# Optimization experiments

Hardware: AMD Instinct MI355X
Metric: run time of the kernel (lower is better)

The kernel has to match this reference:

```python
import jax, jax.numpy as jnp
import numpy as np

B, T, I, H, R, O = 128, 512, 64, 512, 4, 64
NOISE_STD = 0.05
TAU = 0.2


def setup_inputs() -> dict:
    key = jax.random.key(0)
    ks = jax.random.split(key, 16)
    s = 0.08  # xavier-ish scale to keep gates in sane range
    return {
        "u": jax.random.normal(ks[0], (B, T, I), jnp.float32),
        "x0": jnp.zeros((B, H), jnp.float32),
        "noise": jax.random.normal(ks[1], (T, B, H), jnp.float32),
        "W_ir": jax.random.normal(ks[2], (H, I), jnp.float32) * s,
        "b_ir": jax.random.normal(ks[3], (H,), jnp.float32) * s,
        "W_iz": jax.random.normal(ks[4], (H, I), jnp.float32) * s,
        "b_iz": jax.random.normal(ks[5], (H,), jnp.float32) * s,
        "W_ih": jax.random.normal(ks[6], (H, I), jnp.float32) * s,
        "b_ih": jax.random.normal(ks[7], (H,), jnp.float32) * s,
        "N_hr": jax.random.normal(ks[8], (H, R), jnp.float32) * s,
        "M_hr": jax.random.normal(ks[9], (H, R), jnp.float32) * s,
        "N_hz": jax.random.normal(ks[10], (H, R), jnp.float32) * s,
        "M_hz": jax.random.normal(ks[11], (H, R), jnp.float32) * s,
        "N_hh": jax.random.normal(ks[12], (H, R), jnp.float32) * s,
        "M_hh": jax.random.normal(ks[13], (H, R), jnp.float32) * s,
        "W_out": jax.random.normal(ks[14], (O, H), jnp.float32) * s,
        "b_out": jax.random.normal(ks[15], (O,), jnp.float32) * s,
    }


def reference(u, x0, noise, W_ir, b_ir, W_iz, b_iz, W_ih, b_ih,
              N_hr, M_hr, N_hz, M_hz, N_hh, M_hh, W_out, b_out):
    scale = 1.0 / u.shape[-1] * 0 + 1.0 / N_hr.shape[0]  # 1/H (cont mode)
    scale = 1.0 / N_hr.shape[0]
    u_t = jnp.transpose(u, (1, 0, 2))  # [T,B,I]
    # precompute input projections for all steps (same math as per-step Linear)
    ir = jnp.einsum('tbi,hi->tbh', u_t, W_ir) + b_ir
    iz = jnp.einsum('tbi,hi->tbh', u_t, W_iz) + b_iz
    ih = jnp.einsum('tbi,hi->tbh', u_t, W_ih) + b_ih

    def step(x, inp):
        ir_t, iz_t, ih_t, n_t = inp
        hr = (x @ N_hr) @ M_hr.T * scale
        hz = (x @ N_hz) @ M_hz.T * scale
        r = jax.nn.sigmoid(ir_t + hr)
        z = jax.nn.sigmoid(iz_t + hz)
        hh = ((r * x) @ N_hh) @ M_hh.T * scale
        g = jnp.tanh(ih_t + hh)
        rec_x = (1.0 - z) * g + z * x
        x_new = x + NOISE_STD * n_t + TAU * (-x + rec_x)  # cont mode
        return x_new, x_new

    x_last, traj = jax.lax.scan(step, x0, (ir, iz, ih, noise))  # traj: [T,B,H]
    traj = jnp.transpose(traj, (1, 0, 2))  # [B,T,H]
    output = jnp.einsum('bth,oh->bto', traj, W_out) + b_out
    return output, x_last, traj
```

## Files before the change

### kernel.cpp

```cpp
#include <hip/hip_runtime.h>
#include <hip/hip_bf16.h>
#include <stdint.h>

#define Bv 128
#define Tv 512
#define Iv 64
#define Hv 512
#define Ov 64

typedef __attribute__((ext_vector_type(8))) short bv8;
typedef __attribute__((ext_vector_type(4))) float fv4;
typedef __attribute__((ext_vector_type(4))) unsigned uv4;
typedef __attribute__((ext_vector_type(2))) unsigned uv2;
typedef __attribute__((ext_vector_type(8))) unsigned short usv8;

#define LOG2E 1.44269504f
#define TWOLOG2E 2.88539008f

static __device__ __forceinline__ unsigned short f2bf(float f) {
  unsigned u = __builtin_bit_cast(unsigned, f);
  u += 0x7fffu + ((u >> 16) & 1u);
  return (unsigned short)(u >> 16);
}
static __device__ __forceinline__ float bf2f(unsigned short s) {
  return __builtin_bit_cast(float, ((unsigned)s) << 16);
}

template <int CTRL>
static __device__ __forceinline__ float dpp_add(float v) {
  int t = __builtin_amdgcn_update_dpp(0, __builtin_bit_cast(int, v), CTRL, 0xF, 0xF, true);
  return v + __builtin_bit_cast(float, t);
}

static __device__ __forceinline__ float wave_red(float v) {
  v = dpp_add<0xB1>(v);
  v = dpp_add<0x4E>(v);
  v = dpp_add<0x124>(v);
  v = dpp_add<0x128>(v);
  unsigned a = __builtin_bit_cast(unsigned, v);
  uv2 p = __builtin_amdgcn_permlane16_swap(a, a, false, false);
  v = __builtin_bit_cast(float, p[0]) + __builtin_bit_cast(float, p[1]);
  a = __builtin_bit_cast(unsigned, v);
  uv2 q = __builtin_amdgcn_permlane32_swap(a, a, false, false);
  v = __builtin_bit_cast(float, q[0]) + __builtin_bit_cast(float, q[1]);
  return v;
}

__global__ __launch_bounds__(256) void proj_kernel(
    const float* __restrict__ u,
    const float* __restrict__ Wir, const float* __restrict__ bir,
    const float* __restrict__ Wiz, const float* __restrict__ biz,
    const float* __restrict__ Wih, const float* __restrict__ bih,
    unsigned* __restrict__ irz, unsigned short* __restrict__ ihb)
{
  __shared__ __align__(16) unsigned short As[64][72];
  const int bt0 = blockIdx.x * 64;
  const int h0b = blockIdx.y * 64;
  const int tid = threadIdx.x;
  {
    const int r = tid >> 2, ksg = (tid & 3) * 16;
    const float* src = u + (size_t)(bt0 + r) * Iv + ksg;
    unsigned short tmp[16];
#pragma unroll
    for (int i = 0; i < 16; i += 4) {
      float4 v = *(const float4*)(src + i);
      tmp[i] = f2bf(v.x); tmp[i+1] = f2bf(v.y); tmp[i+2] = f2bf(v.z); tmp[i+3] = f2bf(v.w);
    }
    *(uv4*)&As[r][ksg]     = *(uv4*)&tmp[0];
    *(uv4*)&As[r][ksg + 8] = *(uv4*)&tmp[8];
  }
  __syncthreads();
  const int wave = tid >> 6, lane = tid & 63;
  const int n = lane & 15, q = lane >> 4;
  const int h = h0b + wave * 16 + n;
  const float* Wg[3] = {Wir, Wiz, Wih};
  const float SCL[3] = {LOG2E, LOG2E, TWOLOG2E};
  bv8 bfrag[3][2];
#pragma unroll
  for (int g = 0; g < 3; ++g)
#pragma unroll
    for (int ks = 0; ks < 2; ++ks) {
      const float* wp = Wg[g] + (size_t)h * Iv + ks * 32 + q * 8;
      float4 w0 = *(const float4*)wp, w1 = *(const float4*)(wp + 4);
      const float s = SCL[g];
      bv8 f;
      f[0] = (short)f2bf(w0.x * s); f[1] = (short)f2bf(w0.y * s);
      f[2] = (short)f2bf(w0.z * s); f[3] = (short)f2bf(w0.w * s);
      f[4] = (short)f2bf(w1.x * s); f[5] = (short)f2bf(w1.y * s);
      f[6] = (short)f2bf(w1.z * s); f[7] = (short)f2bf(w1.w * s);
      bfrag[g][ks] = f;
    }
  const float bs0 = bir[h] * LOG2E, bs1 = biz[h] * LOG2E, bs2 = bih[h] * TWOLOG2E;
#pragma unroll
  for (int sub = 0; sub < 4; ++sub) {
    bv8 a0 = *(const bv8*)&As[sub * 16 + n][q * 8];
    bv8 a1 = *(const bv8*)&As[sub * 16 + n][32 + q * 8];
    fv4 ar = {0.f,0.f,0.f,0.f}, az = {0.f,0.f,0.f,0.f}, ah = {0.f,0.f,0.f,0.f};
    ar = __builtin_amdgcn_mfma_f32_16x16x32_bf16(a0, bfrag[0][0], ar, 0, 0, 0);
    ar = __builtin_amdgcn_mfma_f32_16x16x32_bf16(a1, bfrag[0][1], ar, 0, 0, 0);
    az = __builtin_amdgcn_mfma_f32_16x16x32_bf16(a0, bfrag[1][0], az, 0, 0, 0);
    az = __builtin_amdgcn_mfma_f32_16x16x32_bf16(a1, bfrag[1][1], az, 0, 0, 0);
    ah = __builtin_amdgcn_mfma_f32_16x16x32_bf16(a0, bfrag[2][0], ah, 0, 0, 0);
    ah = __builtin_amdgcn_mfma_f32_16x16x32_bf16(a1, bfrag[2][1], ah, 0, 0, 0);
#pragma unroll
    for (int j = 0; j < 4; ++j) {
      const int row = bt0 + sub * 16 + q * 4 + j;
      const size_t slot = (size_t)row * Hv + h;
      irz[slot] = ((unsigned)f2bf(az[j] + bs1) << 16) | (unsigned)f2bf(ar[j] + bs0);
      ihb[slot] = f2bf(ah[j] + bs2);
    }
  }
}

struct Buf { uv4 irz0, irz1; usv8 ih; fv4 nz0, nz1; };
#define IRZ(bf, j) ((j) < 4 ? (bf).irz0[(j)] : (bf).irz1[(j) - 4])
#define NZE(bf, j) ((j) < 4 ? (bf).nz0[(j)]  : (bf).nz1[(j) - 4])

__global__ __launch_bounds__(64, 1) void scan_kernel(
    const float* __restrict__ x0, const float* __restrict__ noise,
    const float* __restrict__ Nhr, const float* __restrict__ Mhr,
    const float* __restrict__ Nhz, const float* __restrict__ Mhz,
    const float* __restrict__ Nhh, const float* __restrict__ Mhh,
    unsigned* __restrict__ traj, const unsigned short* __restrict__ ihb,
    float* __restrict__ xlast)
{
  const int b = blockIdx.x, lane = threadIdx.x;
  const int h0 = lane * 8;
  const float scr = (1.0f / 512.0f) * LOG2E;
  const float sch = (1.0f / 512.0f) * TWOLOG2E;
  fv4 nr[8], nz_[8], nh[8], mr[8], mz[8], mh[8];
#pragma unroll
  for (int j = 0; j < 8; ++j) {
    nr[j]  = *(const fv4*)(Nhr + (size_t)(h0 + j) * 4);
    nz_[j] = *(const fv4*)(Nhz + (size_t)(h0 + j) * 4);
    nh[j]  = *(const fv4*)(Nhh + (size_t)(h0 + j) * 4);
    mr[j]  = *(const fv4*)(Mhr + (size_t)(h0 + j) * 4) * scr;
    mz[j]  = *(const fv4*)(Mhz + (size_t)(h0 + j) * 4) * scr;
    mh[j]  = *(const fv4*)(Mhh + (size_t)(h0 + j) * 4) * sch;
  }
#pragma unroll
  for (int j = 0; j < 8; ++j) {
    asm("" : "+a"(nr[j]), "+a"(nz_[j]), "+a"(nh[j]));
    asm("" : "+a"(mr[j]), "+a"(mz[j]), "+a"(mh[j]));
  }
  float x[8];
  {
    fv4 a = *(const fv4*)(x0 + (size_t)b * Hv + h0);
    fv4 c = *(const fv4*)(x0 + (size_t)b * Hv + h0 + 4);
#pragma unroll
    for (int j = 0; j < 4; ++j) { x[j] = a[j]; x[j + 4] = c[j]; }
  }
  const size_t rowbase = (size_t)b * Tv * Hv + h0;
  const size_t nbase = (size_t)b * Hv + h0;
  Buf A, Bb;
  auto LOAD = [&](Buf& bf, int t) {
    const unsigned* p = traj + rowbase + (size_t)t * Hv;
    bf.irz0 = *(const uv4*)p;
    bf.irz1 = *(const uv4*)(p + 4);
    bf.ih = *(const usv8*)(ihb + rowbase + (size_t)t * Hv);
    const float* np = noise + (size_t)t * (Bv * Hv) + nbase;
    bf.nz0 = *(const fv4*)np;
    bf.nz1 = *(const fv4*)(np + 4);
  };
  auto STEP = [&](const Buf& bf, int t) {
    float sr[4] = {0, 0, 0, 0}, sz[4] = {0, 0, 0, 0};
#pragma unroll
    for (int j = 0; j < 8; ++j)
#pragma unroll
      for (int r = 0; r < 4; ++r) {
        sr[r] = fmaf(x[j], nr[j][r], sr[r]);
        sz[r] = fmaf(x[j], nz_[j][r], sz[r]);
      }
#pragma unroll
    for (int r = 0; r < 4; ++r) { sr[r] = wave_red(sr[r]); sz[r] = wave_red(sz[r]); }
    float rx[8], zz[8];
#pragma unroll
    for (int j = 0; j < 8; ++j) {
      float hr = fmaf(sr[3], mr[j][3], fmaf(sr[2], mr[j][2], fmaf(sr[1], mr[j][1], sr[0] * mr[j][0])));
      float hz = fmaf(sz[3], mz[j][3], fmaf(sz[2], mz[j][2], fmaf(sz[1], mz[j][1], sz[0] * mz[j][0])));
      unsigned w = IRZ(bf, j);
      float irv = __builtin_bit_cast(float, w << 16);
      float izv = __builtin_bit_cast(float, w & 0xffff0000u);
      float er = __builtin_amdgcn_exp2f(-(irv + hr));
      float ez = __builtin_amdgcn_exp2f(-(izv + hz));
      rx[j] = __builtin_amdgcn_rcpf(1.0f + er) * x[j];
      zz[j] = __builtin_amdgcn_rcpf(1.0f + ez);
    }
    float sh[4] = {0, 0, 0, 0};
#pragma unroll
    for (int j = 0; j < 8; ++j)
#pragma unroll
      for (int r = 0; r < 4; ++r) sh[r] = fmaf(rx[j], nh[j][r], sh[r]);
#pragma unroll
    for (int r = 0; r < 4; ++r) sh[r] = wave_red(sh[r]);
#pragma unroll
    for (int j = 0; j < 8; ++j) {
      float hh = fmaf(sh[3], mh[j][3], fmaf(sh[2], mh[j][2], fmaf(sh[1], mh[j][1], sh[0] * mh[j][0])));
      float a = fmaxf(bf2f(bf.ih[j]) + hh, -44.0f);
      float e = __builtin_amdgcn_exp2f(-a);
      float g = (1.f - e) * __builtin_amdgcn_rcpf(1.f + e);
      x[j] = x[j] + 0.05f * NZE(bf, j) + 0.2f * (1.f - zz[j]) * (g - x[j]);
    }
    float* op = (float*)(traj + rowbase + (size_t)t * Hv);
    fv4 s0 = {x[0], x[1], x[2], x[3]}, s1 = {x[4], x[5], x[6], x[7]};
    *(fv4*)op = s0;
    *(fv4*)(op + 4) = s1;
  };
  LOAD(A, 0);
  for (int t = 0; t < Tv; t += 2) {
    LOAD(Bb, t + 1);
    STEP(A, t);
    if (t + 2 < Tv) LOAD(A, t + 2);
    STEP(Bb, t + 1);
  }
  {
    fv4 s0 = {x[0], x[1], x[2], x[3]}, s1 = {x[4], x[5], x[6], x[7]};
    *(fv4*)(xlast + nbase) = s0;
    *(fv4*)(xlast + nbase + 4) = s1;
  }
}

__global__ __launch_bounds__(256) void outproj_kernel(
    const float* __restrict__ traj, const float* __restrict__ Wout,
    const float* __restrict__ bout, float* __restrict__ out)
{
  __shared__ __align__(16) unsigned short As[64][40];
  const int bt0 = blockIdx.x * 64;
  const int tid = threadIdx.x;
  const int wave = tid >> 6, lane = tid & 63;
  const int n = lane & 15, q = lane >> 4;
  const int o = wave * 16 + n;
  const float bo = bout[o];
  fv4 acc[4] = {{0.f,0.f,0.f,0.f},{0.f,0.f,0.f,0.f},{0.f,0.f,0.f,0.f},{0.f,0.f,0.f,0.f}};
  const int r = tid >> 2, ksg = (tid & 3) * 8;
  for (int ks = 0; ks < 16; ++ks) {
    __syncthreads();
    {
      const float* src = traj + (size_t)(bt0 + r) * Hv + ks * 32 + ksg;
      float4 v0 = *(const float4*)src, v1 = *(const float4*)(src + 4);
      unsigned short tmp[8];
      tmp[0] = f2bf(v0.x); tmp[1] = f2bf(v0.y); tmp[2] = f2bf(v0.z); tmp[3] = f2bf(v0.w);
      tmp[4] = f2bf(v1.x); tmp[5] = f2bf(v1.y); tmp[6] = f2bf(v1.z); tmp[7] = f2bf(v1.w);
      *(uv4*)&As[r][ksg] = *(uv4*)&tmp[0];
    }
    __syncthreads();
    const float* wp = Wout + (size_t)o * Hv + ks * 32 + q * 8;
    float4 w0 = *(const float4*)wp, w1 = *(const float4*)(wp + 4);
    bv8 bf;
    bf[0] = (short)f2bf(w0.x); bf[1] = (short)f2bf(w0.y);
    bf[2] = (short)f2bf(w0.z); bf[3] = (short)f2bf(w0.w);
    bf[4] = (short)f2bf(w1.x); bf[5] = (short)f2bf(w1.y);
    bf[6] = (short)f2bf(w1.z); bf[7] = (short)f2bf(w1.w);
#pragma unroll
    for (int sub = 0; sub < 4; ++sub) {
      bv8 af = *(const bv8*)&As[sub * 16 + n][q * 8];
      acc[sub] = __builtin_amdgcn_mfma_f32_16x16x32_bf16(af, bf, acc[sub], 0, 0, 0);
    }
  }
#pragma unroll
  for (int sub = 0; sub < 4; ++sub)
#pragma unroll
    for (int j = 0; j < 4; ++j) {
      const int row = bt0 + sub * 16 + q * 4 + j;
      out[(size_t)row * Ov + o] = acc[sub][j] + bo;
    }
}

extern "C" void kernel_launch(void* const* d_in, const int* in_sizes, int n_in,
                              void* d_out, int out_size, void* d_ws, size_t ws_size,
                              hipStream_t stream) {
  const float* u    = (const float*)d_in[0];
  const float* x0   = (const float*)d_in[1];
  const float* noise= (const float*)d_in[2];
  const float* Wir  = (const float*)d_in[3];
  const float* bir  = (const float*)d_in[4];
  const float* Wiz  = (const float*)d_in[5];
  const float* biz  = (const float*)d_in[6];
  const float* Wih  = (const float*)d_in[7];
  const float* bih  = (const float*)d_in[8];
  const float* Nhr  = (const float*)d_in[9];
  const float* Mhr  = (const float*)d_in[10];
  const float* Nhz  = (const float*)d_in[11];
  const float* Mhz  = (const float*)d_in[12];
  const float* Nhh  = (const float*)d_in[13];
  const float* Mhh  = (const float*)d_in[14];
  const float* Wout = (const float*)d_in[15];
  const float* bout = (const float*)d_in[16];

  float* out   = (float*)d_out;
  float* xlast = out + (size_t)Bv * Tv * Ov;
  float* traj  = xlast + (size_t)Bv * Hv;
  unsigned short* ihbuf = (unsigned short*)d_ws;

  proj_kernel<<<dim3(1024, 8, 1), 256, 0, stream>>>(
      u, Wir, bir, Wiz, biz, Wih, bih, (unsigned*)traj, ihbuf);
  scan_kernel<<<dim3(128, 1, 1), 64, 0, stream>>>(
      x0, noise, Nhr, Mhr, Nhz, Mhz, Nhh, Mhh, (unsigned*)traj, ihbuf, xlast);
  outproj_kernel<<<dim3(1024, 1, 1), 256, 0, stream>>>(traj, Wout, bout, out);
}
```

Before: 724.6 us.

## Pack eight batch rows per scan block with shared-memory weights and packed FMAs

The scan kernel now runs 16 blocks of 8 waves, one batch row per wave, instead of 128 single-wave blocks. The low-rank N/M factors move from AGPRs into swizzled shared memory that all waves read. The per-step math uses packed two-wide FMAs, and the negated log2 scales are folded into the projection weights so the exp inputs need no negation. The two sigmoids share one reciprocal, and the tanh clamp is dropped. This concentrates the serial scan on far fewer CUs and adds LDS reads on every step, trading spread across CUs for wave co-residency; removing the clamp risks overflow to inf for large inputs.

```diff
diff --git a/kernel.cpp b/kernel.cpp
--- a/kernel.cpp
+++ b/kernel.cpp
@@ -10,6 +10,7 @@
 
 typedef __attribute__((ext_vector_type(8))) short bv8;
 typedef __attribute__((ext_vector_type(4))) float fv4;
+typedef __attribute__((ext_vector_type(2))) float fv2;
 typedef __attribute__((ext_vector_type(4))) unsigned uv4;
 typedef __attribute__((ext_vector_type(2))) unsigned uv2;
 typedef __attribute__((ext_vector_type(8))) unsigned short usv8;
@@ -24,6 +25,9 @@
 }
 static __device__ __forceinline__ float bf2f(unsigned short s) {
   return __builtin_bit_cast(float, ((unsigned)s) << 16);
+}
+static __device__ __forceinline__ fv2 pkfma(fv2 a, fv2 b, fv2 c) {
+  return __builtin_elementwise_fma(a, b, c);
 }
 
 template <int CTRL>
@@ -74,7 +78,7 @@
   const int n = lane & 15, q = lane >> 4;
   const int h = h0b + wave * 16 + n;
   const float* Wg[3] = {Wir, Wiz, Wih};
-  const float SCL[3] = {LOG2E, LOG2E, TWOLOG2E};
+  const float SCL[3] = {-LOG2E, -LOG2E, -TWOLOG2E};
   bv8 bfrag[3][2];
 #pragma unroll
   for (int g = 0; g < 3; ++g)
@@ -90,7 +94,7 @@
       f[6] = (short)f2bf(w1.z * s); f[7] = (short)f2bf(w1.w * s);
       bfrag[g][ks] = f;
     }
-  const float bs0 = bir[h] * LOG2E, bs1 = biz[h] * LOG2E, bs2 = bih[h] * TWOLOG2E;
+  const float bs0 = bir[h] * -LOG2E, bs1 = biz[h] * -LOG2E, bs2 = bih[h] * -TWOLOG2E;
 #pragma unroll
   for (int sub = 0; sub < 4; ++sub) {
     bv8 a0 = *(const bv8*)&As[sub * 16 + n][q * 8];
@@ -116,7 +120,13 @@
 #define IRZ(bf, j) ((j) < 4 ? (bf).irz0[(j)] : (bf).irz1[(j) - 4])
 #define NZE(bf, j) ((j) < 4 ? (bf).nz0[(j)]  : (bf).nz1[(j) - 4])
 
-__global__ __launch_bounds__(64, 1) void scan_kernel(
+#define OFF_NR 0
+#define OFF_NZ 2048
+#define OFF_NH 4096
+#define OFF_MRZ 6144
+#define OFF_MH2 10240
+
+__global__ __launch_bounds__(512) void scan_kernel(
     const float* __restrict__ x0, const float* __restrict__ noise,
     const float* __restrict__ Nhr, const float* __restrict__ Mhr,
     const float* __restrict__ Nhz, const float* __restrict__ Mhz,
@@ -124,25 +134,49 @@
     unsigned* __restrict__ traj, const unsigned short* __restrict__ ihb,
     float* __restrict__ xlast)
 {
-  const int b = blockIdx.x, lane = threadIdx.x;
+  __shared__ __align__(16) float S[12288];
+  const int tid = threadIdx.x;
+  const int wave = tid >> 6, lane = tid & 63;
+  const int b = blockIdx.x * 8 + wave;
   const int h0 = lane * 8;
-  const float scr = (1.0f / 512.0f) * LOG2E;
-  const float sch = (1.0f / 512.0f) * TWOLOG2E;
-  fv4 nr[8], nz_[8], nh[8], mr[8], mz[8], mh[8];
-#pragma unroll
-  for (int j = 0; j < 8; ++j) {
-    nr[j]  = *(const fv4*)(Nhr + (size_t)(h0 + j) * 4);
-    nz_[j] = *(const fv4*)(Nhz + (size_t)(h0 + j) * 4);
-    nh[j]  = *(const fv4*)(Nhh + (size_t)(h0 + j) * 4);
-    mr[j]  = *(const fv4*)(Mhr + (size_t)(h0 + j) * 4) * scr;
-    mz[j]  = *(const fv4*)(Mhz + (size_t)(h0 + j) * 4) * scr;
-    mh[j]  = *(const fv4*)(Mhh + (size_t)(h0 + j) * 4) * sch;
-  }
-#pragma unroll
-  for (int j = 0; j < 8; ++j) {
-    asm("" : "+a"(nr[j]), "+a"(nz_[j]), "+a"(nh[j]));
-    asm("" : "+a"(mr[j]), "+a"(mz[j]), "+a"(mh[j]));
-  }
+  const int xr = (lane & 7) * 4;
+
+  if (wave == 0) {
+    const float smr = -(1.0f / 512.0f) * LOG2E;
+    const float smh = -(1.0f / 512.0f) * TWOLOG2E;
+#pragma unroll
+    for (int j = 0; j < 8; ++j) {
+      fv4 vr = *(const fv4*)(Nhr + (size_t)(h0 + j) * 4);
+      fv4 vz = *(const fv4*)(Nhz + (size_t)(h0 + j) * 4);
+      fv4 vh = *(const fv4*)(Nhh + (size_t)(h0 + j) * 4);
+      *(fv4*)&S[OFF_NR + lane * 32 + ((j * 4) ^ xr)] = vr;
+      *(fv4*)&S[OFF_NZ + lane * 32 + ((j * 4) ^ xr)] = vz;
+      *(fv4*)&S[OFF_NH + lane * 32 + ((j * 4) ^ xr)] = vh;
+      fv4 mr = *(const fv4*)(Mhr + (size_t)(h0 + j) * 4) * smr;
+      fv4 mz = *(const fv4*)(Mhz + (size_t)(h0 + j) * 4) * smr;
+      fv4 q0 = {mr[0], mz[0], mr[1], mz[1]};
+      fv4 q1 = {mr[2], mz[2], mr[3], mz[3]};
+      *(fv4*)&S[OFF_MRZ + lane * 64 + ((j * 8) ^ xr)]     = q0;
+      *(fv4*)&S[OFF_MRZ + lane * 64 + ((j * 8 + 4) ^ xr)] = q1;
+    }
+#pragma unroll
+    for (int p = 0; p < 4; ++p) {
+      fv4 a = *(const fv4*)(Mhh + (size_t)(h0 + 2 * p) * 4) * smh;
+      fv4 c = *(const fv4*)(Mhh + (size_t)(h0 + 2 * p + 1) * 4) * smh;
+      fv4 q0 = {a[0], c[0], a[1], c[1]};
+      fv4 q1 = {a[2], c[2], a[3], c[3]};
+      *(fv4*)&S[OFF_MH2 + lane * 32 + ((p * 8) ^ xr)]     = q0;
+      *(fv4*)&S[OFF_MH2 + lane * 32 + ((p * 8 + 4) ^ xr)] = q1;
+    }
+  }
+  __syncthreads();
+
+#define NRJ(j)  (*(const fv4*)&S[OFF_NR  + lane * 32 + (((j) * 4) ^ xr)])
+#define NZJ(j)  (*(const fv4*)&S[OFF_NZ  + lane * 32 + (((j) * 4) ^ xr)])
+#define NHJ(j)  (*(const fv4*)&S[OFF_NH  + lane * 32 + (((j) * 4) ^ xr)])
+#define MRZQ(j,h) (*(const fv4*)&S[OFF_MRZ + lane * 64 + ((((j) * 8) + (h) * 4) ^ xr)])
+#define MH2Q(p,h) (*(const fv4*)&S[OFF_MH2 + lane * 32 + ((((p) * 8) + (h) * 4) ^ xr)])
+
   float x[8];
   {
     fv4 a = *(const fv4*)(x0 + (size_t)b * Hv + h0);
@@ -163,43 +197,73 @@
     bf.nz1 = *(const fv4*)(np + 4);
   };
   auto STEP = [&](const Buf& bf, int t) {
-    float sr[4] = {0, 0, 0, 0}, sz[4] = {0, 0, 0, 0};
-#pragma unroll
-    for (int j = 0; j < 8; ++j)
-#pragma unroll
-      for (int r = 0; r < 4; ++r) {
-        sr[r] = fmaf(x[j], nr[j][r], sr[r]);
-        sz[r] = fmaf(x[j], nz_[j][r], sz[r]);
+    fv2 sr01 = {0.f, 0.f}, sr23 = {0.f, 0.f}, sz01 = {0.f, 0.f}, sz23 = {0.f, 0.f};
+#pragma unroll
+    for (int j = 0; j < 8; ++j) {
+      fv4 nrj = NRJ(j), nzj = NZJ(j);
+      fv2 xs = {x[j], x[j]};
+      sr01 = pkfma(xs, fv2{nrj[0], nrj[1]}, sr01);
+      sr23 = pkfma(xs, fv2{nrj[2], nrj[3]}, sr23);
+      sz01 = pkfma(xs, fv2{nzj[0], nzj[1]}, sz01);
+      sz23 = pkfma(xs, fv2{nzj[2], nzj[3]}, sz23);
+    }
+    fv2 srz[4];
+    srz[0] = fv2{wave_red(sr01[0]), wave_red(sz01[0])};
+    srz[1] = fv2{wave_red(sr01[1]), wave_red(sz01[1])};
+    srz[2] = fv2{wave_red(sr23[0]), wave_red(sz23[0])};
+    srz[3] = fv2{wave_red(sr23[1]), wave_red(sz23[1])};
+    float rx[8], w02[8];
+#pragma unroll
+    for (int j = 0; j < 8; ++j) {
+      fv4 q0 = MRZQ(j, 0), q1 = MRZQ(j, 1);
+      fv2 hrz = srz[3] * fv2{q1[2], q1[3]};
+      hrz = pkfma(srz[2], fv2{q1[0], q1[1]}, hrz);
+      hrz = pkfma(srz[1], fv2{q0[2], q0[3]}, hrz);
+      hrz = pkfma(srz[0], fv2{q0[0], q0[1]}, hrz);
+      unsigned w = IRZ(bf, j);
+      float tr = hrz[0] + __builtin_bit_cast(float, w << 16);
+      float tz = hrz[1] + __builtin_bit_cast(float, w & 0xffff0000u);
+      float er = __builtin_amdgcn_exp2f(tr);
+      float ez = __builtin_amdgcn_exp2f(tz);
+      float Ar = 1.0f + er, Az = 1.0f + ez;
+      float R = __builtin_amdgcn_rcpf(Ar * Az);
+      float sigr = R * Az;
+      float sigz = R * Ar;
+      rx[j] = sigr * x[j];
+      w02[j] = fmaf(sigz, -0.2f, 0.2f);
+    }
+    fv2 sh01 = {0.f, 0.f}, sh23 = {0.f, 0.f};
+#pragma unroll
+    for (int j = 0; j < 8; ++j) {
+      fv4 nhj = NHJ(j);
+      fv2 xs = {rx[j], rx[j]};
+      sh01 = pkfma(xs, fv2{nhj[0], nhj[1]}, sh01);
+      sh23 = pkfma(xs, fv2{nhj[2], nhj[3]}, sh23);
+    }
+    fv2 sh2[4];
+    {
+      float s0 = wave_red(sh01[0]), s1 = wave_red(sh01[1]);
+      float s2 = wave_red(sh23[0]), s3 = wave_red(sh23[1]);
+      sh2[0] = fv2{s0, s0}; sh2[1] = fv2{s1, s1};
+      sh2[2] = fv2{s2, s2}; sh2[3] = fv2{s3, s3};
+    }
+#pragma unroll
+    for (int p = 0; p < 4; ++p) {
+      fv4 q0 = MH2Q(p, 0), q1 = MH2Q(p, 1);
+      fv2 hh2 = sh2[3] * fv2{q1[2], q1[3]};
+      hh2 = pkfma(sh2[2], fv2{q1[0], q1[1]}, hh2);
+      hh2 = pkfma(sh2[1], fv2{q0[2], q0[3]}, hh2);
+      hh2 = pkfma(sh2[0], fv2{q0[0], q0[1]}, hh2);
+#pragma unroll
+      for (int k = 0; k < 2; ++k) {
+        const int j = 2 * p + k;
+        float tt = hh2[k] + bf2f(bf.ih[j]);
+        float e = __builtin_amdgcn_exp2f(tt);
+        float g = (1.0f - e) * __builtin_amdgcn_rcpf(1.0f + e);
+        float d = g - x[j];
+        x[j] = fmaf(0.05f, NZE(bf, j), x[j]);
+        x[j] = fmaf(w02[j], d, x[j]);
       }
-#pragma unroll
-    for (int r = 0; r < 4; ++r) { sr[r] = wave_red(sr[r]); sz[r] = wave_red(sz[r]); }
-    float rx[8], zz[8];
-#pragma unroll
-    for (int j = 0; j < 8; ++j) {
-      float hr = fmaf(sr[3], mr[j][3], fmaf(sr[2], mr[j][2], fmaf(sr[1], mr[j][1], sr[0] * mr[j][0])));
-      float hz = fmaf(sz[3], mz[j][3], fmaf(sz[2], mz[j][2], fmaf(sz[1], mz[j][1], sz[0] * mz[j][0])));
-      unsigned w = IRZ(bf, j);
-      float irv = __builtin_bit_cast(float, w << 16);
-      float izv = __builtin_bit_cast(float, w & 0xffff0000u);
-      float er = __builtin_amdgcn_exp2f(-(irv + hr));
-      float ez = __builtin_amdgcn_exp2f(-(izv + hz));
-      rx[j] = __builtin_amdgcn_rcpf(1.0f + er) * x[j];
-      zz[j] = __builtin_amdgcn_rcpf(1.0f + ez);
-    }
-    float sh[4] = {0, 0, 0, 0};
-#pragma unroll
-    for (int j = 0; j < 8; ++j)
-#pragma unroll
-      for (int r = 0; r < 4; ++r) sh[r] = fmaf(rx[j], nh[j][r], sh[r]);
-#pragma unroll
-    for (int r = 0; r < 4; ++r) sh[r] = wave_red(sh[r]);
-#pragma unroll
-    for (int j = 0; j < 8; ++j) {
-      float hh = fmaf(sh[3], mh[j][3], fmaf(sh[2], mh[j][2], fmaf(sh[1], mh[j][1], sh[0] * mh[j][0])));
-      float a = fmaxf(bf2f(bf.ih[j]) + hh, -44.0f);
-      float e = __builtin_amdgcn_exp2f(-a);
-      float g = (1.f - e) * __builtin_amdgcn_rcpf(1.f + e);
-      x[j] = x[j] + 0.05f * NZE(bf, j) + 0.2f * (1.f - zz[j]) * (g - x[j]);
     }
     float* op = (float*)(traj + rowbase + (size_t)t * Hv);
     fv4 s0 = {x[0], x[1], x[2], x[3]}, s1 = {x[4], x[5], x[6], x[7]};
@@ -218,6 +282,11 @@
     *(fv4*)(xlast + nbase) = s0;
     *(fv4*)(xlast + nbase + 4) = s1;
   }
+#undef NRJ
+#undef NZJ
+#undef NHJ
+#undef MRZQ
+#undef MH2Q
 }
 
 __global__ __launch_bounds__(256) void outproj_kernel(
@@ -294,7 +363,7 @@
 
   proj_kernel<<<dim3(1024, 8, 1), 256, 0, stream>>>(
       u, Wir, bir, Wiz, biz, Wih, bih, (unsigned*)traj, ihbuf);
-  scan_kernel<<<dim3(128, 1, 1), 64, 0, stream>>>(
+  scan_kernel<<<dim3(16, 1, 1), 512, 0, stream>>>(
       x0, noise, Nhr, Mhr, Nhz, Mhz, Nhh, Mhh, (unsigned*)traj, ihbuf, xlast);
   outproj_kernel<<<dim3(1024, 1, 1), 256, 0, stream>>>(traj, Wout, bout, out);
 }
```

After: 1.455 ms. +100.8%, slower.
